# Optimization experiments

Hardware: AMD Instinct MI355X
Metric: run time of the kernel (lower is better)

## Reference

```python
import jax, jax.numpy as jnp
import numpy as np

N = 100000
E = 1600000
D = 128
H = 64
C = 10
G = 1024  # number of graphs in the batch


def setup_inputs() -> dict:
    key = jax.random.key(0)
    ks = jax.random.split(key, 12)
    x = jax.random.normal(ks[0], (N, D), dtype=jnp.float32)
    edge_index = jax.random.randint(ks[1], (2, E), 0, N, dtype=jnp.int64)
    batch = jnp.sort(jax.random.randint(ks[2], (N,), 0, G, dtype=jnp.int64))
    def glorot(k, fan_in, fan_out):
        s = jnp.sqrt(6.0 / (fan_in + fan_out))
        return jax.random.uniform(k, (fan_in, fan_out), jnp.float32, -s, s)
    W1 = glorot(ks[3], D, H); b1 = jnp.zeros((H,), jnp.float32)
    W2 = glorot(ks[4], H, H); b2 = jnp.zeros((H,), jnp.float32)
    W3 = glorot(ks[5], H, H); b3 = jnp.zeros((H,), jnp.float32)
    Wl = glorot(ks[6], H, C); bl = jnp.zeros((C,), jnp.float32)
    return {"x": x, "edge_index": edge_index, "batch": batch,
            "W1": W1, "b1": b1, "W2": W2, "b2": b2,
            "W3": W3, "b3": b3, "Wl": Wl, "bl": bl}


def gcn_conv(x, row, col, dinv, W, b):
    # PyG GCNConv: x' = D^-1/2 (A + I) D^-1/2 (x W) + b
    xw = x @ W                                   # (N, H)
    norm = dinv[row] * dinv[col]                 # (E+N,)
    msg = xw[row] * norm[:, None]                # gather + scale
    out = jax.ops.segment_sum(msg, col, num_segments=N)
    return out + b


def reference(x, edge_index, batch, W1, b1, W2, b2, W3, b3, Wl, bl):
    # add self loops once; normalization coefficients shared by all layers
    loop = jnp.arange(N, dtype=edge_index.dtype)
    row = jnp.concatenate([edge_index[0], loop])
    col = jnp.concatenate([edge_index[1], loop])
    deg = jax.ops.segment_sum(jnp.ones_like(col, dtype=x.dtype), col, num_segments=N)
    dinv = jnp.where(deg > 0, jax.lax.rsqrt(deg), 0.0)

    h = gcn_conv(x, row, col, dinv, W1, b1)
    h = gcn_conv(h, row, col, dinv, W2, b2)
    h = gcn_conv(h, row, col, dinv, W3, b3)

    # global mean pool over graphs
    sums = jax.ops.segment_sum(h, batch, num_segments=G)          # (G, H)
    cnts = jax.ops.segment_sum(jnp.ones((N,), h.dtype), batch, num_segments=G)
    pooled = sums / jnp.maximum(cnts, 1.0)[:, None]

    # dropout(p=0.5) is identity in eval mode
    return pooled @ Wl + bl                                        # (G, C)
```

## Files before the change

kernel.cpp:

```cpp
#include <hip/hip_runtime.h>

#define NN 100000
#define EE 1600000
#define DI 128
#define HH 64
#define CO 10
#define PADF 16
#define GG 1024
#define BSH 9
#define BNODES (1 << BSH)
#define NB ((NN + BNODES - 1) / BNODES)
#define TILE 4096
#define NT ((EE + TILE - 1) / TILE)
#define SN (NB * NT)
#define SCB 1024
#define NSB ((SN + SCB - 1) / SCB)
#define BT 256

__global__ __launch_bounds__(256) void k_front(const int* __restrict__ col,
                                               const float* __restrict__ W1, const float* __restrict__ W2,
                                               const float* __restrict__ W3, const float* __restrict__ Wl,
                                               const float* __restrict__ b1, const float* __restrict__ b2,
                                               const float* __restrict__ b3,
                                               const int* __restrict__ batch,
                                               int* __restrict__ cnt, float* __restrict__ Wf,
                                               float* __restrict__ cvec, int* __restrict__ gstart) {
    __shared__ float smem[1280];
    int bid = blockIdx.x, t = threadIdx.x;
    if (bid < NT) {
        int* h = (int*)smem;
        for (int i = t; i < NB; i += 256) h[i] = 0;
        __syncthreads();
        int base = bid * TILE, end = min(base + TILE, EE);
        for (int e = base + t; e < end; e += 256)
            atomicAdd(&h[__builtin_nontemporal_load(&col[e]) >> BSH], 1);
        __syncthreads();
        for (int i = t; i < NB; i += 256) cnt[i * NT + bid] = h[i];
    } else if (bid == NT) {
        float* M3l = smem;
        float* M23l = smem + 640;
        for (int i = t; i < HH * CO; i += 256) {
            int r = i / CO, c = i % CO; float s = 0.f;
            for (int k = 0; k < HH; ++k) s += W3[r * HH + k] * Wl[k * CO + c];
            M3l[i] = s;
        }
        __syncthreads();
        for (int i = t; i < HH * CO; i += 256) {
            int r = i / CO, c = i % CO; float s = 0.f;
            for (int k = 0; k < HH; ++k) s += W2[r * HH + k] * M3l[k * CO + c];
            M23l[i] = s;
        }
        __syncthreads();
        for (int i = t; i < DI * CO; i += 256) {
            int r = i / CO, c = i % CO; float s = 0.f;
            for (int k = 0; k < HH; ++k) s += W1[r * HH + k] * M23l[k * CO + c];
            Wf[i] = s;
        }
        if (t < CO) {
            float s1 = 0.f, s2 = 0.f, s3 = 0.f;
            for (int k = 0; k < HH; ++k) {
                s1 += b1[k] * M23l[k * CO + t];
                s2 += b2[k] * M3l[k * CO + t];
                s3 += b3[k] * Wl[k * CO + t];
            }
            cvec[t] = s1; cvec[CO + t] = s2; cvec[2 * CO + t] = s3;
        }
    } else {
        int g = (bid - NT - 1) * 256 + t;
        if (g <= GG) {
            int lo = 0, hi = NN;
            while (lo < hi) { int mid = (lo + hi) >> 1; if (batch[mid] < g) lo = mid + 1; else hi = mid; }
            gstart[g] = lo;
        }
    }
}

__global__ __launch_bounds__(SCB) void k_scanA(int* __restrict__ a, int* __restrict__ bsum) {
    __shared__ int s[SCB];
    int t = threadIdx.x, idx = blockIdx.x * SCB + t;
    int v = (idx < SN) ? a[idx] : 0;
    s[t] = v;
    __syncthreads();
    for (int off = 1; off < SCB; off <<= 1) {
        int u = (t >= off) ? s[t - off] : 0;
        __syncthreads();
        s[t] += u;
        __syncthreads();
    }
    if (idx < SN) a[idx] = s[t] - v;
    if (t == SCB - 1) bsum[blockIdx.x] = s[t];
}
__global__ __launch_bounds__(SCB) void k_scanC(int* __restrict__ a, const int* __restrict__ bsum) {
    __shared__ int red[SCB];
    int t = threadIdx.x, bid = blockIdx.x;
    int partial = 0;
    for (int i = t; i < bid; i += SCB) partial += bsum[i];
    red[t] = partial;
    __syncthreads();
    for (int off = SCB / 2; off > 0; off >>= 1) {
        if (t < off) red[t] += red[t + off];
        __syncthreads();
    }
    int idx = bid * SCB + t;
    if (idx < SN) a[idx] += red[0];
}

__global__ __launch_bounds__(256) void k_sxw(const int* __restrict__ row, const int* __restrict__ col,
                                             const int* __restrict__ S, unsigned* __restrict__ ebuf,
                                             const float* __restrict__ x, const float* __restrict__ Wf,
                                             float* __restrict__ as_) {
    __shared__ float smf[DI * CO];
    int* smi = (int*)smf;
    int bid = blockIdx.x, t = threadIdx.x;
    if (bid < NT) {
        for (int i = t; i < NB; i += 256) smi[i] = S[i * NT + bid];
        __syncthreads();
        int base = bid * TILE, end = min(base + TILE, EE);
        for (int e = base + t; e < end; e += 256) {
            int c = __builtin_nontemporal_load(&col[e]);
            int r = __builtin_nontemporal_load(&row[e]);
            int pos = atomicAdd(&smi[c >> BSH], 1);
            ebuf[pos] = ((unsigned)r << BSH) | (unsigned)(c & (BNODES - 1));
        }
    } else {
        for (int i = t; i < DI * CO; i += 256) smf[i] = Wf[i];
        __syncthreads();
        int gid = (bid - NT) * 256 + t;
        if (gid >= NN) return;
        int pr = gid >> 1, c0 = (gid & 1) * 5;
        int n0 = 2 * pr, n1 = n0 + 1;
        float a0[5] = {0, 0, 0, 0, 0}, a1[5] = {0, 0, 0, 0, 0};
        const float4* x0 = (const float4*)(x + (size_t)n0 * DI);
        const float4* x1 = (const float4*)(x + (size_t)n1 * DI);
#pragma unroll 4
        for (int d4 = 0; d4 < DI / 4; ++d4) {
            float4 u = x0[d4], v = x1[d4];
            const float* w = &smf[d4 * 4 * CO + c0];
#pragma unroll
            for (int c = 0; c < 5; ++c) {
                float w0 = w[c], w1 = w[CO + c], w2 = w[2 * CO + c], w3 = w[3 * CO + c];
                a0[c] += u.x * w0 + u.y * w1 + u.z * w2 + u.w * w3;
                a1[c] += v.x * w0 + v.y * w1 + v.z * w2 + v.w * w3;
            }
        }
        float* r0 = as_ + (size_t)n0 * PADF + c0;
        float* r1 = as_ + (size_t)n1 * PADF + c0;
#pragma unroll
        for (int c = 0; c < 5; ++c) { r0[c] = a0[c]; r1[c] = a1[c]; }
        if (c0) {
            float* p0 = as_ + (size_t)n0 * PADF;
            float* p1 = as_ + (size_t)n1 * PADF;
            ((float2*)(p0 + 10))[0] = make_float2(0.f, 0.f);
            ((float4*)(p0 + 12))[0] = make_float4(0.f, 0.f, 0.f, 0.f);
            ((float2*)(p1 + 10))[0] = make_float2(0.f, 0.f);
            ((float4*)(p1 + 12))[0] = make_float4(0.f, 0.f, 0.f, 0.f);
        }
    }
}

__global__ __launch_bounds__(256) void k_bsort(const unsigned* __restrict__ ebuf, const int* __restrict__ S,
                                               int* __restrict__ srcIdx, int* __restrict__ rowptr_end,
                                               float* __restrict__ dinv) {
    __shared__ int cnt[BNODES];
    __shared__ int sc[BT];
    __shared__ int ofs[BNODES];
    int t = threadIdx.x;
    int b = blockIdx.x;
    for (int i = t; i < BNODES; i += BT) cnt[i] = 0;
    __syncthreads();
    int beg = S[b * NT];
    int end = (b + 1 < NB) ? S[(b + 1) * NT] : EE;
    for (int e = beg + t; e < end; e += BT)
        atomicAdd(&cnt[__builtin_nontemporal_load(&ebuf[e]) & (BNODES - 1)], 1);
    __syncthreads();
    int v0 = cnt[2 * t], v1 = cnt[2 * t + 1];
    int pair = v0 + v1;
    sc[t] = pair;
    __syncthreads();
    for (int off = 1; off < BT; off <<= 1) {
        int u = (t >= off) ? sc[t - off] : 0;
        __syncthreads();
        sc[t] += u;
        __syncthreads();
    }
    int excl = sc[t] - pair;
    {
        int n0 = (b << BSH) + 2 * t;
        int n1 = n0 + 1;
        if (n0 < NN) {
            dinv[n0] = rsqrtf((float)(v0 + 1));
            rowptr_end[n0] = beg + excl + v0;
        }
        if (n1 < NN) {
            dinv[n1] = rsqrtf((float)(v1 + 1));
            rowptr_end[n1] = beg + excl + v0 + v1;
        }
        ofs[2 * t] = beg + excl;
        ofs[2 * t + 1] = beg + excl + v0;
    }
    __syncthreads();
    for (int e = beg + t; e < end; e += BT) {
        unsigned p = __builtin_nontemporal_load(&ebuf[e]);
        int pos = atomicAdd(&ofs[p & (BNODES - 1)], 1);
        srcIdx[pos] = (int)(p >> BSH);
    }
}

template <int MODE>
__global__ __launch_bounds__(256) void k_gather(const int* __restrict__ rowptr_end,
                                                const int* __restrict__ srcIdx,
                                                const float* __restrict__ src,
                                                const float* __restrict__ dinv,
                                                const float* __restrict__ cvec, int coff,
                                                float* __restrict__ dst) {
    int gid = blockIdx.x * 256 + threadIdx.x;
    int n = gid >> 2;
    int l = threadIdx.x & 3;
    if (n >= NN) return;
    int beg = (n == 0) ? 0 : rowptr_end[n - 1];
    int end = rowptr_end[n];
    float4 acc = make_float4(0.f, 0.f, 0.f, 0.f);
#pragma unroll 4
    for (int e = beg; e < end; ++e) {
        int s = srcIdx[e];
        float4 v = ((const float4*)(src + (size_t)s * PADF))[l];
        if (MODE == 0) {
            float w = dinv[s];
            acc.x += w * v.x; acc.y += w * v.y; acc.z += w * v.z; acc.w += w * v.w;
        } else {
            acc.x += v.x; acc.y += v.y; acc.z += v.z; acc.w += v.w;
        }
    }
    float di = dinv[n];
    float4 sv = ((const float4*)(src + (size_t)n * PADF))[l];
    if (MODE == 0) { sv.x *= di; sv.y *= di; sv.z *= di; sv.w *= di; }
    float cv0, cv1, cv2, cv3;
    {
        int ch = 4 * l;
        cv0 = (ch + 0 < CO) ? cvec[coff + ch + 0] : 0.f;
        cv1 = (ch + 1 < CO) ? cvec[coff + ch + 1] : 0.f;
        cv2 = (ch + 2 < CO) ? cvec[coff + ch + 2] : 0.f;
        cv3 = (ch + 3 < CO) ? cvec[coff + ch + 3] : 0.f;
    }
    float4 o;
    o.x = di * (acc.x + sv.x) + cv0;
    o.y = di * (acc.y + sv.y) + cv1;
    o.z = di * (acc.z + sv.z) + cv2;
    o.w = di * (acc.w + sv.w) + cv3;
    if (MODE != 2) { o.x *= di; o.y *= di; o.z *= di; o.w *= di; }
    ((float4*)(dst + (size_t)n * PADF))[l] = o;
}

__global__ __launch_bounds__(64) void k_pool(const float* __restrict__ h,
                                             const int* __restrict__ gstart,
                                             const float* __restrict__ bl,
                                             float* __restrict__ out) {
    int g = blockIdx.x;
    int beg = gstart[g], end = gstart[g + 1];
    int l = threadIdx.x;
    float acc[CO];
#pragma unroll
    for (int c = 0; c < CO; ++c) acc[c] = 0.f;
    for (int n = beg + l; n < end; n += 64) {
        const float* sp = h + (size_t)n * PADF;
        float4 a = ((const float4*)sp)[0];
        float4 b = ((const float4*)sp)[1];
        float2 c2 = ((const float2*)(sp + 8))[0];
        acc[0] += a.x; acc[1] += a.y; acc[2] += a.z; acc[3] += a.w;
        acc[4] += b.x; acc[5] += b.y; acc[6] += b.z; acc[7] += b.w;
        acc[8] += c2.x; acc[9] += c2.y;
    }
#pragma unroll
    for (int m = 1; m < 64; m <<= 1) {
#pragma unroll
        for (int c = 0; c < CO; ++c) acc[c] += __shfl_xor(acc[c], m, 64);
    }
    if (l == 0) {
        float cf = fmaxf((float)(end - beg), 1.f);
#pragma unroll
        for (int c = 0; c < CO; ++c) out[(size_t)g * CO + c] = acc[c] / cf + bl[c];
    }
}

extern "C" void kernel_launch(void* const* d_in, const int* in_sizes, int n_in,
                              void* d_out, int out_size, void* d_ws, size_t ws_size,
                              hipStream_t stream) {
    const float* x    = (const float*)d_in[0];
    const int*   ei   = (const int*)d_in[1];
    const int*   batch= (const int*)d_in[2];
    const float* W1   = (const float*)d_in[3];
    const float* b1   = (const float*)d_in[4];
    const float* W2   = (const float*)d_in[5];
    const float* b2   = (const float*)d_in[6];
    const float* W3   = (const float*)d_in[7];
    const float* b3   = (const float*)d_in[8];
    const float* Wl   = (const float*)d_in[9];
    const float* bl   = (const float*)d_in[10];
    float* out = (float*)d_out;

    const int* row = ei;
    const int* col = ei + EE;

    float* ws = (float*)d_ws;
    size_t off = 0;
    auto alloc = [&](size_t elems) { size_t cur = off; off += (elems + 63) & ~(size_t)63; return cur; };
    float*    Wf      = ws + alloc(DI * CO);
    float*    cvec    = ws + alloc(3 * CO);
    float*    dinv    = ws + alloc(NN);
    int*      S       = (int*)(ws + alloc(SN));
    int*      bsum    = (int*)(ws + alloc(NSB + 64));
    unsigned* ebuf    = (unsigned*)(ws + alloc(EE));
    int*      srcIdx  = (int*)(ws + alloc(EE));
    int*      rowptr  = (int*)(ws + alloc(NN));
    float*    as_     = ws + alloc((size_t)NN * PADF);
    float*    bbuf    = ws + alloc((size_t)NN * PADF);
    int*      gstart  = (int*)(ws + alloc(GG + 1));
    (void)ws_size; (void)in_sizes; (void)n_in; (void)out_size;

    int gNL = ((NN * 4) + BT - 1) / BT;
    int gFront = NT + 1 + (GG + 1 + BT - 1) / BT;
    int gSxw = NT + (NN + BT - 1) / BT;

    hipLaunchKernelGGL(k_front,    dim3(gFront), dim3(BT), 0, stream,
                       col, W1, W2, W3, Wl, b1, b2, b3, batch, S, Wf, cvec, gstart);
    hipLaunchKernelGGL(k_scanA,    dim3(NSB), dim3(SCB), 0, stream, S, bsum);
    hipLaunchKernelGGL(k_scanC,    dim3(NSB), dim3(SCB), 0, stream, S, bsum);
    hipLaunchKernelGGL(k_sxw,      dim3(gSxw), dim3(BT), 0, stream, row, col, S, ebuf, x, Wf, as_);
    hipLaunchKernelGGL(k_bsort,    dim3(NB),  dim3(BT), 0, stream, ebuf, S, srcIdx, rowptr, dinv);

    hipLaunchKernelGGL((k_gather<0>), dim3(gNL), dim3(BT), 0, stream, rowptr, srcIdx, as_,  dinv, cvec, 0,      bbuf);
    hipLaunchKernelGGL((k_gather<1>), dim3(gNL), dim3(BT), 0, stream, rowptr, srcIdx, bbuf, dinv, cvec, CO,     as_);
    hipLaunchKernelGGL((k_gather<2>), dim3(gNL), dim3(BT), 0, stream, rowptr, srcIdx, as_,  dinv, cvec, 2 * CO, bbuf);

    hipLaunchKernelGGL(k_pool, dim3(GG), dim3(64), 0, stream, bbuf, gstart, bl, out);
}
```

Baseline: 264.2 us.

## Split gather edge loop across two thread groups and widen sort buckets

The neighbor gather now assigns eight threads per node: two groups of four each take alternate edges and combine partial sums with a cross-lane shuffle before one group writes the output. The bucket sort uses 1024-node buckets instead of 512, with each thread scanning four counters. The aim is more memory-level parallelism in the gather and fewer, larger sort blocks. The risks are half the threads idling in the epilogue, and fewer sort blocks lowering occupancy in the sort.

```diff
diff --git a/kernel.cpp b/kernel.cpp
--- a/kernel.cpp
+++ b/kernel.cpp
@@ -7,7 +7,7 @@
 #define CO 10
 #define PADF 16
 #define GG 1024
-#define BSH 9
+#define BSH 10
 #define BNODES (1 << BSH)
 #define NB ((NN + BNODES - 1) / BNODES)
 #define TILE 4096
@@ -173,9 +173,9 @@
     for (int e = beg + t; e < end; e += BT)
         atomicAdd(&cnt[__builtin_nontemporal_load(&ebuf[e]) & (BNODES - 1)], 1);
     __syncthreads();
-    int v0 = cnt[2 * t], v1 = cnt[2 * t + 1];
-    int pair = v0 + v1;
-    sc[t] = pair;
+    int v0 = cnt[4 * t], v1 = cnt[4 * t + 1], v2 = cnt[4 * t + 2], v3 = cnt[4 * t + 3];
+    int quad = v0 + v1 + v2 + v3;
+    sc[t] = quad;
     __syncthreads();
     for (int off = 1; off < BT; off <<= 1) {
         int u = (t >= off) ? sc[t - off] : 0;
@@ -183,20 +183,20 @@
         sc[t] += u;
         __syncthreads();
     }
-    int excl = sc[t] - pair;
+    int excl = sc[t] - quad;
     {
-        int n0 = (b << BSH) + 2 * t;
-        int n1 = n0 + 1;
-        if (n0 < NN) {
-            dinv[n0] = rsqrtf((float)(v0 + 1));
-            rowptr_end[n0] = beg + excl + v0;
-        }
-        if (n1 < NN) {
-            dinv[n1] = rsqrtf((float)(v1 + 1));
-            rowptr_end[n1] = beg + excl + v0 + v1;
-        }
-        ofs[2 * t] = beg + excl;
-        ofs[2 * t + 1] = beg + excl + v0;
+        int nbase = (b << BSH) + 4 * t;
+        int starts[4] = {excl, excl + v0, excl + v0 + v1, excl + v0 + v1 + v2};
+        int vs[4] = {v0, v1, v2, v3};
+#pragma unroll
+        for (int k = 0; k < 4; ++k) {
+            int n = nbase + k;
+            if (n < NN) {
+                dinv[n] = rsqrtf((float)(vs[k] + 1));
+                rowptr_end[n] = beg + starts[k] + vs[k];
+            }
+            ofs[4 * t + k] = beg + starts[k];
+        }
     }
     __syncthreads();
     for (int e = beg + t; e < end; e += BT) {
@@ -214,14 +214,16 @@
                                                 const float* __restrict__ cvec, int coff,
                                                 float* __restrict__ dst) {
     int gid = blockIdx.x * 256 + threadIdx.x;
-    int n = gid >> 2;
-    int l = threadIdx.x & 3;
+    int n = gid >> 3;
+    int lane8 = threadIdx.x & 7;
+    int q = lane8 >> 2;
+    int l = lane8 & 3;
     if (n >= NN) return;
     int beg = (n == 0) ? 0 : rowptr_end[n - 1];
     int end = rowptr_end[n];
     float4 acc = make_float4(0.f, 0.f, 0.f, 0.f);
 #pragma unroll 4
-    for (int e = beg; e < end; ++e) {
+    for (int e = beg + q; e < end; e += 2) {
         int s = srcIdx[e];
         float4 v = ((const float4*)(src + (size_t)s * PADF))[l];
         if (MODE == 0) {
@@ -231,24 +233,30 @@
             acc.x += v.x; acc.y += v.y; acc.z += v.z; acc.w += v.w;
         }
     }
-    float di = dinv[n];
-    float4 sv = ((const float4*)(src + (size_t)n * PADF))[l];
-    if (MODE == 0) { sv.x *= di; sv.y *= di; sv.z *= di; sv.w *= di; }
-    float cv0, cv1, cv2, cv3;
-    {
-        int ch = 4 * l;
-        cv0 = (ch + 0 < CO) ? cvec[coff + ch + 0] : 0.f;
-        cv1 = (ch + 1 < CO) ? cvec[coff + ch + 1] : 0.f;
-        cv2 = (ch + 2 < CO) ? cvec[coff + ch + 2] : 0.f;
-        cv3 = (ch + 3 < CO) ? cvec[coff + ch + 3] : 0.f;
-    }
-    float4 o;
-    o.x = di * (acc.x + sv.x) + cv0;
-    o.y = di * (acc.y + sv.y) + cv1;
-    o.z = di * (acc.z + sv.z) + cv2;
-    o.w = di * (acc.w + sv.w) + cv3;
-    if (MODE != 2) { o.x *= di; o.y *= di; o.z *= di; o.w *= di; }
-    ((float4*)(dst + (size_t)n * PADF))[l] = o;
+    acc.x += __shfl_xor(acc.x, 4, 64);
+    acc.y += __shfl_xor(acc.y, 4, 64);
+    acc.z += __shfl_xor(acc.z, 4, 64);
+    acc.w += __shfl_xor(acc.w, 4, 64);
+    if (q == 0) {
+        float di = dinv[n];
+        float4 sv = ((const float4*)(src + (size_t)n * PADF))[l];
+        if (MODE == 0) { sv.x *= di; sv.y *= di; sv.z *= di; sv.w *= di; }
+        float cv0, cv1, cv2, cv3;
+        {
+            int ch = 4 * l;
+            cv0 = (ch + 0 < CO) ? cvec[coff + ch + 0] : 0.f;
+            cv1 = (ch + 1 < CO) ? cvec[coff + ch + 1] : 0.f;
+            cv2 = (ch + 2 < CO) ? cvec[coff + ch + 2] : 0.f;
+            cv3 = (ch + 3 < CO) ? cvec[coff + ch + 3] : 0.f;
+        }
+        float4 o;
+        o.x = di * (acc.x + sv.x) + cv0;
+        o.y = di * (acc.y + sv.y) + cv1;
+        o.z = di * (acc.z + sv.z) + cv2;
+        o.w = di * (acc.w + sv.w) + cv3;
+        if (MODE != 2) { o.x *= di; o.y *= di; o.z *= di; o.w *= di; }
+        ((float4*)(dst + (size_t)n * PADF))[l] = o;
+    }
 }
 
 __global__ __launch_bounds__(64) void k_pool(const float* __restrict__ h,
@@ -317,7 +325,7 @@
     int*      gstart  = (int*)(ws + alloc(GG + 1));
     (void)ws_size; (void)in_sizes; (void)n_in; (void)out_size;
 
-    int gNL = ((NN * 4) + BT - 1) / BT;
+    int gNL = ((NN * 8) + BT - 1) / BT;
     int gFront = NT + 1 + (GG + 1 + BT - 1) / BT;
     int gSxw = NT + (NN + BT - 1) / BT;
 
```

Result: slower. 281.2 us (+6.4%).
